# Kernel tuning notes

Measured on AMD Instinct MI355X. Metric: run time of the kernel, lower is better.

The kernel has to match this reference:

```python
import jax, jax.numpy as jnp
import numpy as np

N = 50000      # nodes
E = 800000     # edges (before self loops)
IN_DIM = 128
HID = 16
HEADS = 8
OUT_DIM = 40
NEG_SLOPE = 0.2


def setup_inputs() -> dict:
    key = jax.random.key(0)
    ks = jax.random.split(key, 10)
    x = jax.random.normal(ks[0], (N, IN_DIM), jnp.float32)
    edge_index = jax.random.randint(ks[1], (2, E), 0, N, dtype=jnp.int32)
    # layer 1: GATConv(IN_DIM, HID, heads=HEADS, concat=True)
    W1 = jax.random.normal(ks[2], (IN_DIM, HEADS * HID), jnp.float32) / np.sqrt(IN_DIM).astype(np.float32)
    att_src1 = jax.random.normal(ks[3], (HEADS, HID), jnp.float32) * 0.1
    att_dst1 = jax.random.normal(ks[4], (HEADS, HID), jnp.float32) * 0.1
    bias1 = jnp.zeros((HEADS * HID,), jnp.float32)
    # layer 2: GATConv(HEADS*HID, OUT_DIM, heads=1, concat=False)
    W2 = jax.random.normal(ks[5], (HEADS * HID, OUT_DIM), jnp.float32) / np.sqrt(HEADS * HID).astype(np.float32)
    att_src2 = jax.random.normal(ks[6], (1, OUT_DIM), jnp.float32) * 0.1
    att_dst2 = jax.random.normal(ks[7], (1, OUT_DIM), jnp.float32) * 0.1
    bias2 = jnp.zeros((OUT_DIM,), jnp.float32)
    return {"x": x, "W1": W1, "att_src1": att_src1, "att_dst1": att_dst1, "bias1": bias1,
            "W2": W2, "att_src2": att_src2, "att_dst2": att_dst2, "bias2": bias2,
            "edge_index": edge_index}


def gat_conv(x, src, dst, W, att_src, att_dst, bias, heads, dim, concat, num_nodes):
    # h: [N, H, D]
    h = (x @ W).reshape(num_nodes, heads, dim)
    a_src = jnp.sum(h * att_src, axis=-1)  # [N, H]
    a_dst = jnp.sum(h * att_dst, axis=-1)  # [N, H]
    e = a_src[src] + a_dst[dst]            # [E', H]
    e = jnp.where(e > 0, e, NEG_SLOPE * e)  # leaky_relu
    # segment softmax over edges sharing the same target node
    m = jax.ops.segment_max(e, dst, num_segments=num_nodes)  # [N, H]
    e = jnp.exp(e - m[dst])
    s = jax.ops.segment_sum(e, dst, num_segments=num_nodes)  # [N, H]
    alpha = e / (s[dst] + 1e-16)            # [E', H]
    msg = h[src] * alpha[:, :, None]        # [E', H, D]
    out = jax.ops.segment_sum(msg, dst, num_segments=num_nodes)  # [N, H, D]
    if concat:
        out = out.reshape(num_nodes, heads * dim)
    else:
        out = out.mean(axis=1)
    return out + bias


def reference(x, W1, att_src1, att_dst1, bias1, W2, att_src2, att_dst2, bias2, edge_index):
    # add self loops (PyG GATConv default)
    loop = jnp.arange(N, dtype=edge_index.dtype)
    src = jnp.concatenate([edge_index[0], loop])
    dst = jnp.concatenate([edge_index[1], loop])
    # eval mode: dropout (p=0.6) is identity
    h = gat_conv(x, src, dst, W1, att_src1, att_dst1, bias1, HEADS, HID, True, N)
    h = jax.nn.elu(h)
    out = gat_conv(h, src, dst, W2, att_src2, att_dst2, bias2, 1, OUT_DIM, False, N)
    return jax.nn.log_softmax(out, axis=1)
```

## Files before the change

kernel.cpp:

```cpp
#include <hip/hip_runtime.h>
#include <math.h>

#define IN_DIM 128
#define HEADS 8
#define HID 16
#define OUT_DIM 40
#define NEG 0.2f
#define NSLICE 8

typedef short bf16x8 __attribute__((ext_vector_type(8)));
typedef float f32x4 __attribute__((ext_vector_type(4)));

__device__ __forceinline__ unsigned short f32_to_bf16_rne(float v) {
  unsigned u = __float_as_uint(v);
  return (unsigned short)((u + 0x7FFFu + ((u >> 16) & 1u)) >> 16);
}


__global__ __launch_bounds__(1024) void scanA_k(const int* __restrict__ deg, int* __restrict__ rp,
                                                int* __restrict__ bsum, int n) {
  __shared__ int wsum[16];
  int tid = threadIdx.x;
  int i = blockIdx.x * 1024 + tid;
  int lane = tid & 63, w = tid >> 6;
  int v = (i < n) ? deg[i] : 0;
  int x = v;
  #pragma unroll
  for (int off = 1; off < 64; off <<= 1) {
    int y = __shfl_up(x, off);
    if (lane >= off) x += y;
  }
  if (lane == 63) wsum[w] = x;
  __syncthreads();
  if (tid < 16) {
    int s = wsum[tid];
    #pragma unroll
    for (int off = 1; off < 16; off <<= 1) {
      int y = __shfl_up(s, off);
      if (tid >= off) s += y;
    }
    wsum[tid] = s;
  }
  __syncthreads();
  int woff = (w == 0) ? 0 : wsum[w - 1];
  if (i < n) rp[i] = woff + x - v;
  if (tid == 0) bsum[blockIdx.x] = wsum[15];
}

__global__ __launch_bounds__(1024) void scanB_k(int* __restrict__ bsum, int nb,
                                                int* __restrict__ rp, int n) {
  __shared__ int wsum[16];
  int tid = threadIdx.x;
  int lane = tid & 63, w = tid >> 6;
  int v = (tid < nb) ? bsum[tid] : 0;
  int x = v;
  #pragma unroll
  for (int off = 1; off < 64; off <<= 1) {
    int y = __shfl_up(x, off);
    if (lane >= off) x += y;
  }
  if (lane == 63) wsum[w] = x;
  __syncthreads();
  if (tid < 16) {
    int s = wsum[tid];
    #pragma unroll
    for (int off = 1; off < 16; off <<= 1) {
      int y = __shfl_up(s, off);
      if (tid >= off) s += y;
    }
    wsum[tid] = s;
  }
  __syncthreads();
  int woff = (w == 0) ? 0 : wsum[w - 1];
  if (tid < nb) bsum[tid] = woff + x - v;
  if (tid == 0) rp[n] = wsum[15];
}

__global__ __launch_bounds__(1024) void scanC_k(int* __restrict__ rp, const int* __restrict__ bsum,
                                                int* __restrict__ cnt, int n) {
  int i = blockIdx.x * 1024 + threadIdx.x;
  if (i < n) {
    int v = rp[i] + bsum[blockIdx.x];
    rp[i] = v;
    cnt[i] = v;
  }
}

__global__ void scatter_k(const int* __restrict__ ei, int E0, int N, int snode,
                          int* __restrict__ cnt, int* __restrict__ csr_src) {
  int b = blockIdx.x;
  int slice = b & (NSLICE - 1);
  int e = (b >> 3) * 256 + threadIdx.x;
  int EP = E0 + N;
  if (e >= EP) return;
  int d = (e < E0) ? ei[E0 + e] : (e - E0);
  if (d / snode != slice) return;
  int s = (e < E0) ? ei[e] : d;
  int pos = atomicAdd(&cnt[d], 1);
  csr_src[pos] = s;
}

__global__ void prep_k(const float* __restrict__ W1, const float* __restrict__ as1,
                       const float* __restrict__ ad1, const float* __restrict__ W2,
                       const float* __restrict__ as2, const float* __restrict__ ad2,
                       unsigned short* __restrict__ whi, unsigned short* __restrict__ wlo,
                       unsigned short* __restrict__ w2p, int* __restrict__ deg, int N) {
  int t = blockIdx.x * 256 + threadIdx.x;
  if (t < N) deg[t] = 0;
  if (t < 18432) {
    int j = t & 7, lane = (t >> 3) & 63, kc = (t >> 9) & 3, ct = t >> 11;
    int k = kc * 32 + (lane >> 4) * 8 + j;
    int col = lane & 15;
    float v;
    if (ct < 8) {
      v = W1[k * 128 + ct * 16 + col];
    } else {
      int h = col & 7;
      const float* att = (col < 8) ? as1 : ad1;
      float s = 0.f;
      #pragma unroll
      for (int d = 0; d < 16; ++d) s += W1[k * 128 + h * 16 + d] * att[h * 16 + d];
      v = s;
    }
    unsigned u = __float_as_uint(v);
    unsigned hi = (u + 0x7FFFu + ((u >> 16) & 1u)) >> 16;
    float rem = v - __uint_as_float(hi << 16);
    unsigned ur = __float_as_uint(rem);
    unsigned lo = (ur + 0x7FFFu + ((ur >> 16) & 1u)) >> 16;
    whi[t] = (unsigned short)hi;
    wlo[t] = (unsigned short)lo;
  } else if (t < 18432 + 6144) {
    int u2 = t - 18432;
    int j = u2 & 7, lane = (u2 >> 3) & 63, kc = (u2 >> 9) & 3, ct = u2 >> 11;
    int k = kc * 32 + (lane >> 4) * 8 + j;
    int col = ct * 16 + (lane & 15);
    float v;
    if (col < OUT_DIM) {
      v = W2[k * OUT_DIM + col];
    } else if (col < 42) {
      const float* att = (col == OUT_DIM) ? as2 : ad2;
      float s = 0.f;
      #pragma unroll 8
      for (int d = 0; d < OUT_DIM; ++d) s += W2[k * OUT_DIM + d] * att[d];
      v = s;
    } else {
      v = 0.f;
    }
    w2p[u2] = f32_to_bf16_rne(v);
  }
}

__global__ __launch_bounds__(256) void gemm1_hist_k(
    const float* __restrict__ x, const unsigned short* __restrict__ whi,
    const unsigned short* __restrict__ wlo,
    unsigned short* __restrict__ h1, float* __restrict__ a1s, float* __restrict__ a1d,
    int N, int G1,
    const int* __restrict__ ei, int E0, int snode, int* __restrict__ deg) {
  if ((int)blockIdx.x >= G1) {
    int b = blockIdx.x - G1;
    int slice = b & (NSLICE - 1);
    int e = (b >> 3) * 256 + threadIdx.x;
    int EP = E0 + N;
    if (e >= EP) return;
    int d = (e < E0) ? ei[E0 + e] : (e - E0);
    if (d / snode == slice) atomicAdd(&deg[d], 1);
    return;
  }
  int w = threadIdx.x >> 6, lane = threadIdx.x & 63;
  int quad = lane >> 4, l15 = lane & 15;
  int row = blockIdx.x * 64 + w * 16 + l15;
  int rowc = (row < N) ? row : (N - 1);

  f32x4 acc[9];
  #pragma unroll
  for (int t = 0; t < 9; ++t) acc[t] = (f32x4){0.f, 0.f, 0.f, 0.f};

  const float* xr = x + (size_t)rowc * 128 + quad * 8;
  #pragma unroll
  for (int kc = 0; kc < 4; ++kc) {
    f32x4 a0 = *reinterpret_cast<const f32x4*>(xr + kc * 32);
    f32x4 a1 = *reinterpret_cast<const f32x4*>(xr + kc * 32 + 4);
    float av[8] = {a0.x, a0.y, a0.z, a0.w, a1.x, a1.y, a1.z, a1.w};
    bf16x8 ahi, alo;
    #pragma unroll
    for (int j = 0; j < 8; ++j) {
      unsigned u = __float_as_uint(av[j]);
      unsigned hi = (u + 0x7FFFu + ((u >> 16) & 1u)) >> 16;
      float rem = av[j] - __uint_as_float(hi << 16);
      unsigned ur = __float_as_uint(rem);
      unsigned lo = (ur + 0x7FFFu + ((ur >> 16) & 1u)) >> 16;
      ahi[j] = (short)hi;
      alo[j] = (short)lo;
    }
    #pragma unroll
    for (int ct = 0; ct < 9; ++ct) {
      bf16x8 bh = *reinterpret_cast<const bf16x8*>(whi + ((size_t)(ct * 4 + kc) * 64 + lane) * 8);
      bf16x8 bl = *reinterpret_cast<const bf16x8*>(wlo + ((size_t)(ct * 4 + kc) * 64 + lane) * 8);
      acc[ct] = __builtin_amdgcn_mfma_f32_16x16x32_bf16(ahi, bh, acc[ct], 0, 0, 0);
      acc[ct] = __builtin_amdgcn_mfma_f32_16x16x32_bf16(ahi, bl, acc[ct], 0, 0, 0);
      acc[ct] = __builtin_amdgcn_mfma_f32_16x16x32_bf16(alo, bh, acc[ct], 0, 0, 0);
    }
  }
  int rbase = blockIdx.x * 64 + w * 16 + quad * 4;
  #pragma unroll
  for (int reg = 0; reg < 4; ++reg) {
    int r = rbase + reg;
    if (r < N) {
      #pragma unroll
      for (int ct = 0; ct < 8; ++ct)
        h1[(size_t)r * 128 + ct * 16 + l15] = f32_to_bf16_rne(acc[ct][reg]);
      float v = acc[8][reg];
      if (l15 < 8) a1s[r * 8 + l15] = v;
      else         a1d[r * 8 + (l15 - 8)] = v;
    }
  }
}

__global__ __launch_bounds__(256) void agg1_k(
    const int* __restrict__ row_ptr, const int* __restrict__ csr_src,
    const float* __restrict__ a1s, const float* __restrict__ a1d,
    const unsigned* __restrict__ h1u, const float* __restrict__ bias1,
    unsigned* __restrict__ vrowp, int N) {
  int wid = threadIdx.x >> 6;
  int lane = threadIdx.x & 63;
  int n = blockIdx.x * 4 + wid;

  __shared__ __align__(16) float wls_s[4][8 * 132];
  __shared__ __align__(16) int   srcs_s[4][128];

  if (n >= N) return;
  float* wls  = wls_s[wid];
  int*   srcs = srcs_s[wid];

  int rs = row_ptr[n], re = row_ptr[n + 1];
  int deg = re - rs;
  int h = lane >> 3;

  float accx = 0.f, accy = 0.f, inv;

  if (deg <= 128) {
    for (int i0 = lane; i0 < deg; i0 += 64) srcs[i0] = csr_src[rs + i0];
    int slot = lane >> 3, hw = lane & 7;
    float adn = a1d[n * 8 + hw];
    float sw = 0.f;
    for (int i0 = 0; i0 < deg; i0 += 16) {
      int ia = i0 + slot, ib = i0 + 8 + slot;
      bool va = ia < deg, vb = ib < deg;
      int sa = srcs[va ? ia : 0];
      int sb = srcs[vb ? ib : 0];
      float ea = a1s[sa * 8 + hw] + adn;
      float eb = a1s[sb * 8 + hw] + adn;
      ea = fmaxf(ea, NEG * ea);
      eb = fmaxf(eb, NEG * eb);
      float wa = va ? __expf(ea) : 0.f;
      float wb = vb ? __expf(eb) : 0.f;
      sw += wa + wb;
      if (va) wls[hw * 132 + ia] = wa;
      if (vb) wls[hw * 132 + ib] = wb;
    }
    sw += __shfl_xor(sw, 8);
    sw += __shfl_xor(sw, 16);
    sw += __shfl_xor(sw, 32);
    inv = __shfl(1.f / (sw + 1e-16f), h);

    const float* wh = wls + h * 132;
    int i = 0;
    for (; i + 16 <= deg; i += 16) {
      int4 sa = *reinterpret_cast<const int4*>(srcs + i);
      int4 sb = *reinterpret_cast<const int4*>(srcs + i + 4);
      int4 sc = *reinterpret_cast<const int4*>(srcs + i + 8);
      int4 sd = *reinterpret_cast<const int4*>(srcs + i + 12);
      float4 wa = *reinterpret_cast<const float4*>(wh + i);
      float4 wb = *reinterpret_cast<const float4*>(wh + i + 4);
      float4 wc = *reinterpret_cast<const float4*>(wh + i + 8);
      float4 wd = *reinterpret_cast<const float4*>(wh + i + 12);
      unsigned u0 = h1u[(size_t)sa.x * 64 + lane];
      unsigned u1 = h1u[(size_t)sa.y * 64 + lane];
      unsigned u2 = h1u[(size_t)sa.z * 64 + lane];
      unsigned u3 = h1u[(size_t)sa.w * 64 + lane];
      unsigned u4 = h1u[(size_t)sb.x * 64 + lane];
      unsigned u5 = h1u[(size_t)sb.y * 64 + lane];
      unsigned u6 = h1u[(size_t)sb.z * 64 + lane];
      unsigned u7 = h1u[(size_t)sb.w * 64 + lane];
      unsigned u8 = h1u[(size_t)sc.x * 64 + lane];
      unsigned u9 = h1u[(size_t)sc.y * 64 + lane];
      unsigned uA = h1u[(size_t)sc.z * 64 + lane];
      unsigned uB = h1u[(size_t)sc.w * 64 + lane];
      unsigned uC = h1u[(size_t)sd.x * 64 + lane];
      unsigned uD = h1u[(size_t)sd.y * 64 + lane];
      unsigned uE = h1u[(size_t)sd.z * 64 + lane];
      unsigned uF = h1u[(size_t)sd.w * 64 + lane];
      accx += wa.x * __uint_as_float(u0 << 16) + wa.y * __uint_as_float(u1 << 16)
            + wa.z * __uint_as_float(u2 << 16) + wa.w * __uint_as_float(u3 << 16)
            + wb.x * __uint_as_float(u4 << 16) + wb.y * __uint_as_float(u5 << 16)
            + wb.z * __uint_as_float(u6 << 16) + wb.w * __uint_as_float(u7 << 16)
            + wc.x * __uint_as_float(u8 << 16) + wc.y * __uint_as_float(u9 << 16)
            + wc.z * __uint_as_float(uA << 16) + wc.w * __uint_as_float(uB << 16)
            + wd.x * __uint_as_float(uC << 16) + wd.y * __uint_as_float(uD << 16)
            + wd.z * __uint_as_float(uE << 16) + wd.w * __uint_as_float(uF << 16);
      accy += wa.x * __uint_as_float(u0 & 0xFFFF0000u) + wa.y * __uint_as_float(u1 & 0xFFFF0000u)
            + wa.z * __uint_as_float(u2 & 0xFFFF0000u) + wa.w * __uint_as_float(u3 & 0xFFFF0000u)
            + wb.x * __uint_as_float(u4 & 0xFFFF0000u) + wb.y * __uint_as_float(u5 & 0xFFFF0000u)
            + wb.z * __uint_as_float(u6 & 0xFFFF0000u) + wb.w * __uint_as_float(u7 & 0xFFFF0000u)
            + wc.x * __uint_as_float(u8 & 0xFFFF0000u) + wc.y * __uint_as_float(u9 & 0xFFFF0000u)
            + wc.z * __uint_as_float(uA & 0xFFFF0000u) + wc.w * __uint_as_float(uB & 0xFFFF0000u)
            + wd.x * __uint_as_float(uC & 0xFFFF0000u) + wd.y * __uint_as_float(uD & 0xFFFF0000u)
            + wd.z * __uint_as_float(uE & 0xFFFF0000u) + wd.w * __uint_as_float(uF & 0xFFFF0000u);
    }
    for (; i + 4 <= deg; i += 4) {
      int4 sa = *reinterpret_cast<const int4*>(srcs + i);
      float4 wa = *reinterpret_cast<const float4*>(wh + i);
      unsigned u0 = h1u[(size_t)sa.x * 64 + lane];
      unsigned u1 = h1u[(size_t)sa.y * 64 + lane];
      unsigned u2 = h1u[(size_t)sa.z * 64 + lane];
      unsigned u3 = h1u[(size_t)sa.w * 64 + lane];
      accx += wa.x * __uint_as_float(u0 << 16) + wa.y * __uint_as_float(u1 << 16)
            + wa.z * __uint_as_float(u2 << 16) + wa.w * __uint_as_float(u3 << 16);
      accy += wa.x * __uint_as_float(u0 & 0xFFFF0000u) + wa.y * __uint_as_float(u1 & 0xFFFF0000u)
            + wa.z * __uint_as_float(u2 & 0xFFFF0000u) + wa.w * __uint_as_float(u3 & 0xFFFF0000u);
    }
    for (; i < deg; ++i) {
      int s = srcs[i];
      float w = wh[i];
      unsigned u = h1u[(size_t)s * 64 + lane];
      accx += w * __uint_as_float(u << 16);
      accy += w * __uint_as_float(u & 0xFFFF0000u);
    }
  } else {
    float adn = a1d[n * 8 + h];
    float sw = 0.f;
    for (int i = rs; i < re; ++i) {
      int s = csr_src[i];
      float e = a1s[s * 8 + h] + adn;
      e = fmaxf(e, NEG * e);
      float w = __expf(e);
      unsigned u = h1u[(size_t)s * 64 + lane];
      sw += w;
      accx += w * __uint_as_float(u << 16);
      accy += w * __uint_as_float(u & 0xFFFF0000u);
    }
    inv = 1.f / (sw + 1e-16f);
  }

  float2 b = *reinterpret_cast<const float2*>(bias1 + 2 * lane);
  float vx = accx * inv + b.x;
  float vy = accy * inv + b.y;
  vx = (vx > 0.f) ? vx : (__expf(vx) - 1.f);
  vy = (vy > 0.f) ? vy : (__expf(vy) - 1.f);
  unsigned packed = (unsigned)f32_to_bf16_rne(vx) | ((unsigned)f32_to_bf16_rne(vy) << 16);
  vrowp[(size_t)n * 64 + lane] = packed;
}

__global__ __launch_bounds__(256) void gemm2_mfma_k(
    const unsigned short* __restrict__ vrow, const unsigned short* __restrict__ w2p,
    unsigned short* __restrict__ h2, float* __restrict__ a2s, float* __restrict__ a2d, int N) {
  int w = threadIdx.x >> 6, lane = threadIdx.x & 63;
  int quad = lane >> 4, l15 = lane & 15;
  int row = blockIdx.x * 64 + w * 16 + l15;
  int rowc = (row < N) ? row : (N - 1);

  f32x4 acc[3];
  #pragma unroll
  for (int t = 0; t < 3; ++t) acc[t] = (f32x4){0.f, 0.f, 0.f, 0.f};

  const unsigned short* vr = vrow + (size_t)rowc * 128 + quad * 8;
  #pragma unroll
  for (int kc = 0; kc < 4; ++kc) {
    bf16x8 a = *reinterpret_cast<const bf16x8*>(vr + kc * 32);
    #pragma unroll
    for (int ct = 0; ct < 3; ++ct) {
      bf16x8 bfrag = *reinterpret_cast<const bf16x8*>(w2p + ((size_t)(ct * 4 + kc) * 64 + lane) * 8);
      acc[ct] = __builtin_amdgcn_mfma_f32_16x16x32_bf16(a, bfrag, acc[ct], 0, 0, 0);
    }
  }
  int rbase = blockIdx.x * 64 + w * 16 + quad * 4;
  #pragma unroll
  for (int reg = 0; reg < 4; ++reg) {
    int r = rbase + reg;
    if (r < N) {
      #pragma unroll
      for (int ct = 0; ct < 3; ++ct) {
        int col = ct * 16 + l15;
        float v = acc[ct][reg];
        if (col < OUT_DIM)       h2[(size_t)r * 64 + col] = f32_to_bf16_rne(v);
        else if (col == OUT_DIM) a2s[r] = v;
        else if (col == 41)      a2d[r] = v;
      }
    }
  }
}

__global__ __launch_bounds__(256) void agg2_k(
    const int* __restrict__ row_ptr, const int* __restrict__ csr_src,
    const float* __restrict__ a2s, const float* __restrict__ a2d,
    const unsigned short* __restrict__ h2, const float* __restrict__ bias2,
    float* __restrict__ out, int N) {
  int wid = threadIdx.x >> 6;
  int lane = threadIdx.x & 63;
  int n = blockIdx.x * 4 + wid;

  __shared__ __align__(16) float wls_s[4][128];
  __shared__ __align__(16) int   srcs_s[4][128];

  if (n >= N) return;
  float* wls  = wls_s[wid];
  int*   srcs = srcs_s[wid];

  int rs = row_ptr[n], re = row_ptr[n + 1];
  int deg = re - rs;
  float adn = a2d[n];
  bool act = lane < OUT_DIM;
  float acc = 0.f, inv;

  if (deg <= 128) {
    for (int i0 = lane; i0 < deg; i0 += 64) srcs[i0] = csr_src[rs + i0];
    int ia = lane, ib = lane + 64;
    bool va = ia < deg, vb = ib < deg;
    int sa = srcs[va ? ia : 0];
    int sb = srcs[vb ? ib : 0];
    float ea = a2s[sa] + adn;
    float eb = a2s[sb] + adn;
    ea = fmaxf(ea, NEG * ea);
    eb = fmaxf(eb, NEG * eb);
    float wa = va ? __expf(ea) : 0.f;
    float wb = vb ? __expf(eb) : 0.f;
    float sw = wa + wb;
    if (va) wls[ia] = wa;
    if (vb) wls[ib] = wb;
    #pragma unroll
    for (int off = 32; off > 0; off >>= 1) sw += __shfl_xor(sw, off);
    inv = 1.f / (sw + 1e-16f);

    int i = 0;
    for (; i + 16 <= deg; i += 16) {
      int4 s0 = *reinterpret_cast<const int4*>(srcs + i);
      int4 s1 = *reinterpret_cast<const int4*>(srcs + i + 4);
      int4 s2 = *reinterpret_cast<const int4*>(srcs + i + 8);
      int4 s3 = *reinterpret_cast<const int4*>(srcs + i + 12);
      float4 w0 = *reinterpret_cast<const float4*>(wls + i);
      float4 w1 = *reinterpret_cast<const float4*>(wls + i + 4);
      float4 w2 = *reinterpret_cast<const float4*>(wls + i + 8);
      float4 w3 = *reinterpret_cast<const float4*>(wls + i + 12);
      unsigned g0 = h2[(size_t)s0.x * 64 + lane];
      unsigned g1 = h2[(size_t)s0.y * 64 + lane];
      unsigned g2 = h2[(size_t)s0.z * 64 + lane];
      unsigned g3 = h2[(size_t)s0.w * 64 + lane];
      unsigned g4 = h2[(size_t)s1.x * 64 + lane];
      unsigned g5 = h2[(size_t)s1.y * 64 + lane];
      unsigned g6 = h2[(size_t)s1.z * 64 + lane];
      unsigned g7 = h2[(size_t)s1.w * 64 + lane];
      unsigned g8 = h2[(size_t)s2.x * 64 + lane];
      unsigned g9 = h2[(size_t)s2.y * 64 + lane];
      unsigned gA = h2[(size_t)s2.z * 64 + lane];
      unsigned gB = h2[(size_t)s2.w * 64 + lane];
      unsigned gC = h2[(size_t)s3.x * 64 + lane];
      unsigned gD = h2[(size_t)s3.y * 64 + lane];
      unsigned gE = h2[(size_t)s3.z * 64 + lane];
      unsigned gF = h2[(size_t)s3.w * 64 + lane];
      acc += w0.x * __uint_as_float(g0 << 16) + w0.y * __uint_as_float(g1 << 16)
           + w0.z * __uint_as_float(g2 << 16) + w0.w * __uint_as_float(g3 << 16)
           + w1.x * __uint_as_float(g4 << 16) + w1.y * __uint_as_float(g5 << 16)
           + w1.z * __uint_as_float(g6 << 16) + w1.w * __uint_as_float(g7 << 16)
           + w2.x * __uint_as_float(g8 << 16) + w2.y * __uint_as_float(g9 << 16)
           + w2.z * __uint_as_float(gA << 16) + w2.w * __uint_as_float(gB << 16)
           + w3.x * __uint_as_float(gC << 16) + w3.y * __uint_as_float(gD << 16)
           + w3.z * __uint_as_float(gE << 16) + w3.w * __uint_as_float(gF << 16);
    }
    for (; i + 4 <= deg; i += 4) {
      int4 s0 = *reinterpret_cast<const int4*>(srcs + i);
      float4 w0 = *reinterpret_cast<const float4*>(wls + i);
      unsigned g0 = h2[(size_t)s0.x * 64 + lane];
      unsigned g1 = h2[(size_t)s0.y * 64 + lane];
      unsigned g2 = h2[(size_t)s0.z * 64 + lane];
      unsigned g3 = h2[(size_t)s0.w * 64 + lane];
      acc += w0.x * __uint_as_float(g0 << 16) + w0.y * __uint_as_float(g1 << 16)
           + w0.z * __uint_as_float(g2 << 16) + w0.w * __uint_as_float(g3 << 16);
    }
    for (; i < deg; ++i) {
      int s = srcs[i];
      float w = wls[i];
      unsigned g = h2[(size_t)s * 64 + lane];
      acc += w * __uint_as_float(g << 16);
    }
  } else {
    float sw = 0.f;
    for (int i = rs; i < re; ++i) {
      int s = csr_src[i];
      float e = a2s[s] + adn;
      e = fmaxf(e, NEG * e);
      float w = __expf(e);
      sw += w;
      unsigned g = h2[(size_t)s * 64 + lane];
      acc += w * __uint_as_float(g << 16);
    }
    inv = 1.f / (sw + 1e-16f);
  }

  float v = act ? (acc * inv + bias2[lane]) : -1e30f;
  float vm = v;
  #pragma unroll
  for (int off = 32; off > 0; off >>= 1) vm = fmaxf(vm, __shfl_xor(vm, off));
  float ex = act ? __expf(v - vm) : 0.f;
  float es = ex;
  #pragma unroll
  for (int off = 32; off > 0; off >>= 1) es += __shfl_xor(es, off);
  if (act) out[(size_t)n * OUT_DIM + lane] = v - vm - __logf(es);
}


extern "C" void kernel_launch(void* const* d_in, const int* in_sizes, int n_in,
                              void* d_out, int out_size, void* d_ws, size_t ws_size,
                              hipStream_t stream) {
  const float* x   = (const float*)d_in[0];
  const float* W1  = (const float*)d_in[1];
  const float* as1 = (const float*)d_in[2];
  const float* ad1 = (const float*)d_in[3];
  const float* b1  = (const float*)d_in[4];
  const float* W2  = (const float*)d_in[5];
  const float* as2 = (const float*)d_in[6];
  const float* ad2 = (const float*)d_in[7];
  const float* b2  = (const float*)d_in[8];
  const int*   ei  = (const int*)d_in[9];
  int N  = in_sizes[0] / IN_DIM;
  int E0 = in_sizes[9] / 2;
  int EP = E0 + N;
  int snode = (N + NSLICE - 1) / NSLICE;
  float* out = (float*)d_out;

  char* ws = (char*)d_ws;
  size_t off = 0;
  auto alloc = [&](size_t bytes) {
    char* p = ws + off;
    off += (bytes + 255) & ~size_t(255);
    return p;
  };
  unsigned short* h1   = (unsigned short*)alloc((size_t)N * 128 * 2);
  float* a1s  = (float*)alloc((size_t)N * 8 * 4);
  float* a1d  = (float*)alloc((size_t)N * 8 * 4);
  unsigned*       vrow = (unsigned*)alloc((size_t)N * 64 * 4);
  unsigned short* h2   = (unsigned short*)alloc((size_t)N * 64 * 2);
  float* a2s  = (float*)alloc((size_t)N * 4);
  float* a2d  = (float*)alloc((size_t)N * 4);
  int*   deg  = (int*)alloc((size_t)N * 4);
  int*   cnt  = (int*)alloc((size_t)N * 4);
  int*   rp   = (int*)alloc((size_t)(N + 4) * 4);
  int*   bsum = (int*)alloc((size_t)1024 * 4);
  int*   csr  = (int*)alloc((size_t)EP * 4);
  unsigned short* whi = (unsigned short*)alloc((size_t)18432 * 2);
  unsigned short* wlo = (unsigned short*)alloc((size_t)18432 * 2);
  unsigned short* w2p = (unsigned short*)alloc((size_t)6144 * 2);

  int nb = (N + 1023) / 1024;
  int nchunk = (EP + 255) / 256;
  int G1 = (N + 63) / 64;
  prep_k<<<(N + 255) / 256, 256, 0, stream>>>(W1, as1, ad1, W2, as2, ad2, whi, wlo, w2p, deg, N);
  gemm1_hist_k<<<G1 + nchunk * NSLICE, 256, 0, stream>>>(x, whi, wlo, h1, a1s, a1d, N, G1,
                                                         ei, E0, snode, deg);
  scanA_k<<<nb, 1024, 0, stream>>>(deg, rp, bsum, N);
  scanB_k<<<1, 1024, 0, stream>>>(bsum, nb, rp, N);
  scanC_k<<<nb, 1024, 0, stream>>>(rp, bsum, cnt, N);
  scatter_k<<<nchunk * NSLICE, 256, 0, stream>>>(ei, E0, N, snode, cnt, csr);
  agg1_k<<<(N + 3) / 4, 256, 0, stream>>>(rp, csr, a1s, a1d, (const unsigned*)h1, b1, vrow, N);
  gemm2_mfma_k<<<(N + 63) / 64, 256, 0, stream>>>((const unsigned short*)vrow, w2p, h2, a2s, a2d, N);
  agg2_k<<<(N + 3) / 4, 256, 0, stream>>>(rp, csr, a2s, a2d, h2, b2, out, N);
}
```

Measured before the change: 258.0 us.

## Reschedule CSR build: histogram in prep, fuse scans, scatter alongside gemm1, pair-gather agg2

```diff
diff --git a/kernel.cpp b/kernel.cpp
--- a/kernel.cpp
+++ b/kernel.cpp
@@ -7,6 +7,7 @@
 #define OUT_DIM 40
 #define NEG 0.2f
 #define NSLICE 8
+#define PREP_BLOCKS 96
 
 typedef short bf16x8 __attribute__((ext_vector_type(8)));
 typedef float f32x4 __attribute__((ext_vector_type(4)));
@@ -16,97 +17,24 @@
   return (unsigned short)((u + 0x7FFFu + ((u >> 16) & 1u)) >> 16);
 }
 
-
-__global__ __launch_bounds__(1024) void scanA_k(const int* __restrict__ deg, int* __restrict__ rp,
-                                                int* __restrict__ bsum, int n) {
-  __shared__ int wsum[16];
-  int tid = threadIdx.x;
-  int i = blockIdx.x * 1024 + tid;
-  int lane = tid & 63, w = tid >> 6;
-  int v = (i < n) ? deg[i] : 0;
-  int x = v;
-  #pragma unroll
-  for (int off = 1; off < 64; off <<= 1) {
-    int y = __shfl_up(x, off);
-    if (lane >= off) x += y;
-  }
-  if (lane == 63) wsum[w] = x;
-  __syncthreads();
-  if (tid < 16) {
-    int s = wsum[tid];
-    #pragma unroll
-    for (int off = 1; off < 16; off <<= 1) {
-      int y = __shfl_up(s, off);
-      if (tid >= off) s += y;
-    }
-    wsum[tid] = s;
-  }
-  __syncthreads();
-  int woff = (w == 0) ? 0 : wsum[w - 1];
-  if (i < n) rp[i] = woff + x - v;
-  if (tid == 0) bsum[blockIdx.x] = wsum[15];
-}
-
-__global__ __launch_bounds__(1024) void scanB_k(int* __restrict__ bsum, int nb,
-                                                int* __restrict__ rp, int n) {
-  __shared__ int wsum[16];
-  int tid = threadIdx.x;
-  int lane = tid & 63, w = tid >> 6;
-  int v = (tid < nb) ? bsum[tid] : 0;
-  int x = v;
-  #pragma unroll
-  for (int off = 1; off < 64; off <<= 1) {
-    int y = __shfl_up(x, off);
-    if (lane >= off) x += y;
-  }
-  if (lane == 63) wsum[w] = x;
-  __syncthreads();
-  if (tid < 16) {
-    int s = wsum[tid];
-    #pragma unroll
-    for (int off = 1; off < 16; off <<= 1) {
-      int y = __shfl_up(s, off);
-      if (tid >= off) s += y;
-    }
-    wsum[tid] = s;
-  }
-  __syncthreads();
-  int woff = (w == 0) ? 0 : wsum[w - 1];
-  if (tid < nb) bsum[tid] = woff + x - v;
-  if (tid == 0) rp[n] = wsum[15];
-}
-
-__global__ __launch_bounds__(1024) void scanC_k(int* __restrict__ rp, const int* __restrict__ bsum,
-                                                int* __restrict__ cnt, int n) {
-  int i = blockIdx.x * 1024 + threadIdx.x;
-  if (i < n) {
-    int v = rp[i] + bsum[blockIdx.x];
-    rp[i] = v;
-    cnt[i] = v;
-  }
-}
-
-__global__ void scatter_k(const int* __restrict__ ei, int E0, int N, int snode,
-                          int* __restrict__ cnt, int* __restrict__ csr_src) {
-  int b = blockIdx.x;
-  int slice = b & (NSLICE - 1);
-  int e = (b >> 3) * 256 + threadIdx.x;
-  int EP = E0 + N;
-  if (e >= EP) return;
-  int d = (e < E0) ? ei[E0 + e] : (e - E0);
-  if (d / snode != slice) return;
-  int s = (e < E0) ? ei[e] : d;
-  int pos = atomicAdd(&cnt[d], 1);
-  csr_src[pos] = s;
-}
-
-__global__ void prep_k(const float* __restrict__ W1, const float* __restrict__ as1,
-                       const float* __restrict__ ad1, const float* __restrict__ W2,
-                       const float* __restrict__ as2, const float* __restrict__ ad2,
-                       unsigned short* __restrict__ whi, unsigned short* __restrict__ wlo,
-                       unsigned short* __restrict__ w2p, int* __restrict__ deg, int N) {
+__global__ void prep_hist_k(const float* __restrict__ W1, const float* __restrict__ as1,
+                            const float* __restrict__ ad1, const float* __restrict__ W2,
+                            const float* __restrict__ as2, const float* __restrict__ ad2,
+                            unsigned short* __restrict__ whi, unsigned short* __restrict__ wlo,
+                            unsigned short* __restrict__ w2p,
+                            const int* __restrict__ ei, int E0, int N, int snode,
+                            int* __restrict__ deg) {
+  if ((int)blockIdx.x >= PREP_BLOCKS) {
+    int b = blockIdx.x - PREP_BLOCKS;
+    int slice = b & (NSLICE - 1);
+    int e = (b >> 3) * 256 + threadIdx.x;
+    int EP = E0 + N;
+    if (e >= EP) return;
+    int d = (e < E0) ? ei[E0 + e] : (e - E0);
+    if (d / snode == slice) atomicAdd(&deg[d], 1);
+    return;
+  }
   int t = blockIdx.x * 256 + threadIdx.x;
-  if (t < N) deg[t] = 0;
   if (t < 18432) {
     int j = t & 7, lane = (t >> 3) & 63, kc = (t >> 9) & 3, ct = t >> 11;
     int k = kc * 32 + (lane >> 4) * 8 + j;
@@ -150,12 +78,82 @@
   }
 }
 
-__global__ __launch_bounds__(256) void gemm1_hist_k(
+__global__ __launch_bounds__(1024) void scanA_k(const int* __restrict__ deg, int* __restrict__ rp,
+                                                int* __restrict__ bsum, int n) {
+  __shared__ int wsum[16];
+  int tid = threadIdx.x;
+  int i = blockIdx.x * 1024 + tid;
+  int lane = tid & 63, w = tid >> 6;
+  int v = (i < n) ? deg[i] : 0;
+  int x = v;
+  #pragma unroll
+  for (int off = 1; off < 64; off <<= 1) {
+    int y = __shfl_up(x, off);
+    if (lane >= off) x += y;
+  }
+  if (lane == 63) wsum[w] = x;
+  __syncthreads();
+  if (tid < 16) {
+    int s = wsum[tid];
+    #pragma unroll
+    for (int off = 1; off < 16; off <<= 1) {
+      int y = __shfl_up(s, off);
+      if (tid >= off) s += y;
+    }
+    wsum[tid] = s;
+  }
+  __syncthreads();
+  int woff = (w == 0) ? 0 : wsum[w - 1];
+  if (i < n) rp[i] = woff + x - v;
+  if (tid == 0) bsum[blockIdx.x] = wsum[15];
+}
+
+__global__ __launch_bounds__(1024) void scanBC_k(const int* __restrict__ bsum, int nb,
+                                                 int* __restrict__ rp, int* __restrict__ cnt, int n) {
+  __shared__ int wsum[16];
+  __shared__ int offs[1025];
+  int tid = threadIdx.x;
+  int lane = tid & 63, w = tid >> 6;
+  int v = (tid < nb) ? bsum[tid] : 0;
+  int x = v;
+  #pragma unroll
+  for (int off = 1; off < 64; off <<= 1) {
+    int y = __shfl_up(x, off);
+    if (lane >= off) x += y;
+  }
+  if (lane == 63) wsum[w] = x;
+  __syncthreads();
+  if (tid < 16) {
+    int s = wsum[tid];
+    #pragma unroll
+    for (int off = 1; off < 16; off <<= 1) {
+      int y = __shfl_up(s, off);
+      if (tid >= off) s += y;
+    }
+    wsum[tid] = s;
+  }
+  __syncthreads();
+  int woff = (w == 0) ? 0 : wsum[w - 1];
+  if (tid < nb) offs[tid + 1] = woff + x;
+  if (tid == 0) offs[0] = 0;
+  __syncthreads();
+  int add = offs[blockIdx.x];
+  int i = blockIdx.x * 1024 + tid;
+  if (i < n) {
+    int val = rp[i] + add;
+    rp[i] = val;
+    cnt[i] = val;
+  }
+  if (blockIdx.x == 0 && tid == 0) rp[n] = offs[nb];
+}
+
+__global__ __launch_bounds__(256) void gemm1_scatter_k(
     const float* __restrict__ x, const unsigned short* __restrict__ whi,
     const unsigned short* __restrict__ wlo,
     unsigned short* __restrict__ h1, float* __restrict__ a1s, float* __restrict__ a1d,
     int N, int G1,
-    const int* __restrict__ ei, int E0, int snode, int* __restrict__ deg) {
+    const int* __restrict__ ei, int E0, int snode,
+    int* __restrict__ cnt, int* __restrict__ csr_src) {
   if ((int)blockIdx.x >= G1) {
     int b = blockIdx.x - G1;
     int slice = b & (NSLICE - 1);
@@ -163,7 +161,10 @@
     int EP = E0 + N;
     if (e >= EP) return;
     int d = (e < E0) ? ei[E0 + e] : (e - E0);
-    if (d / snode == slice) atomicAdd(&deg[d], 1);
+    if (d / snode != slice) return;
+    int s = (e < E0) ? ei[e] : d;
+    int pos = atomicAdd(&cnt[d], 1);
+    csr_src[pos] = s;
     return;
   }
   int w = threadIdx.x >> 6, lane = threadIdx.x & 63;
@@ -393,7 +394,7 @@
 __global__ __launch_bounds__(256) void agg2_k(
     const int* __restrict__ row_ptr, const int* __restrict__ csr_src,
     const float* __restrict__ a2s, const float* __restrict__ a2d,
-    const unsigned short* __restrict__ h2, const float* __restrict__ bias2,
+    const unsigned* __restrict__ h2u, const float* __restrict__ bias2,
     float* __restrict__ out, int N) {
   int wid = threadIdx.x >> 6;
   int lane = threadIdx.x & 63;
@@ -409,8 +410,9 @@
   int rs = row_ptr[n], re = row_ptr[n + 1];
   int deg = re - rs;
   float adn = a2d[n];
-  bool act = lane < OUT_DIM;
-  float acc = 0.f, inv;
+  int pair = lane >> 5;
+  int c32  = lane & 31;
+  float accx = 0.f, accy = 0.f, inv;
 
   if (deg <= 128) {
     for (int i0 = lane; i0 < deg; i0 += 64) srcs[i0] = csr_src[rs + i0];
@@ -433,78 +435,62 @@
 
     int i = 0;
     for (; i + 16 <= deg; i += 16) {
-      int4 s0 = *reinterpret_cast<const int4*>(srcs + i);
-      int4 s1 = *reinterpret_cast<const int4*>(srcs + i + 4);
-      int4 s2 = *reinterpret_cast<const int4*>(srcs + i + 8);
-      int4 s3 = *reinterpret_cast<const int4*>(srcs + i + 12);
-      float4 w0 = *reinterpret_cast<const float4*>(wls + i);
-      float4 w1 = *reinterpret_cast<const float4*>(wls + i + 4);
-      float4 w2 = *reinterpret_cast<const float4*>(wls + i + 8);
-      float4 w3 = *reinterpret_cast<const float4*>(wls + i + 12);
-      unsigned g0 = h2[(size_t)s0.x * 64 + lane];
-      unsigned g1 = h2[(size_t)s0.y * 64 + lane];
-      unsigned g2 = h2[(size_t)s0.z * 64 + lane];
-      unsigned g3 = h2[(size_t)s0.w * 64 + lane];
-      unsigned g4 = h2[(size_t)s1.x * 64 + lane];
-      unsigned g5 = h2[(size_t)s1.y * 64 + lane];
-      unsigned g6 = h2[(size_t)s1.z * 64 + lane];
-      unsigned g7 = h2[(size_t)s1.w * 64 + lane];
-      unsigned g8 = h2[(size_t)s2.x * 64 + lane];
-      unsigned g9 = h2[(size_t)s2.y * 64 + lane];
-      unsigned gA = h2[(size_t)s2.z * 64 + lane];
-      unsigned gB = h2[(size_t)s2.w * 64 + lane];
-      unsigned gC = h2[(size_t)s3.x * 64 + lane];
-      unsigned gD = h2[(size_t)s3.y * 64 + lane];
-      unsigned gE = h2[(size_t)s3.z * 64 + lane];
-      unsigned gF = h2[(size_t)s3.w * 64 + lane];
-      acc += w0.x * __uint_as_float(g0 << 16) + w0.y * __uint_as_float(g1 << 16)
-           + w0.z * __uint_as_float(g2 << 16) + w0.w * __uint_as_float(g3 << 16)
-           + w1.x * __uint_as_float(g4 << 16) + w1.y * __uint_as_float(g5 << 16)
-           + w1.z * __uint_as_float(g6 << 16) + w1.w * __uint_as_float(g7 << 16)
-           + w2.x * __uint_as_float(g8 << 16) + w2.y * __uint_as_float(g9 << 16)
-           + w2.z * __uint_as_float(gA << 16) + w2.w * __uint_as_float(gB << 16)
-           + w3.x * __uint_as_float(gC << 16) + w3.y * __uint_as_float(gD << 16)
-           + w3.z * __uint_as_float(gE << 16) + w3.w * __uint_as_float(gF << 16);
-    }
-    for (; i + 4 <= deg; i += 4) {
-      int4 s0 = *reinterpret_cast<const int4*>(srcs + i);
-      float4 w0 = *reinterpret_cast<const float4*>(wls + i);
-      unsigned g0 = h2[(size_t)s0.x * 64 + lane];
-      unsigned g1 = h2[(size_t)s0.y * 64 + lane];
-      unsigned g2 = h2[(size_t)s0.z * 64 + lane];
-      unsigned g3 = h2[(size_t)s0.w * 64 + lane];
-      acc += w0.x * __uint_as_float(g0 << 16) + w0.y * __uint_as_float(g1 << 16)
-           + w0.z * __uint_as_float(g2 << 16) + w0.w * __uint_as_float(g3 << 16);
-    }
-    for (; i < deg; ++i) {
-      int s = srcs[i];
-      float w = wls[i];
-      unsigned g = h2[(size_t)s * 64 + lane];
-      acc += w * __uint_as_float(g << 16);
+      #pragma unroll
+      for (int j = 0; j < 8; ++j) {
+        int idx = i + 2 * j + pair;
+        int s = srcs[idx];
+        float w = wls[idx];
+        unsigned g = h2u[(size_t)s * 32 + c32];
+        accx += w * __uint_as_float(g << 16);
+        accy += w * __uint_as_float(g & 0xFFFF0000u);
+      }
+    }
+    for (; i < deg; i += 2) {
+      int idx = i + pair;
+      bool val = idx < deg;
+      int s = srcs[val ? idx : 0];
+      float w = val ? wls[idx] : 0.f;
+      unsigned g = h2u[(size_t)s * 32 + c32];
+      accx += w * __uint_as_float(g << 16);
+      accy += w * __uint_as_float(g & 0xFFFF0000u);
     }
   } else {
     float sw = 0.f;
-    for (int i = rs; i < re; ++i) {
-      int s = csr_src[i];
+    for (int i = rs; i < re; i += 2) {
+      int idx = i + pair;
+      bool val = idx < re;
+      int s = csr_src[val ? idx : rs];
       float e = a2s[s] + adn;
       e = fmaxf(e, NEG * e);
-      float w = __expf(e);
+      float w = val ? __expf(e) : 0.f;
       sw += w;
-      unsigned g = h2[(size_t)s * 64 + lane];
-      acc += w * __uint_as_float(g << 16);
-    }
-    inv = 1.f / (sw + 1e-16f);
-  }
-
-  float v = act ? (acc * inv + bias2[lane]) : -1e30f;
-  float vm = v;
+      unsigned g = h2u[(size_t)s * 32 + c32];
+      accx += w * __uint_as_float(g << 16);
+      accy += w * __uint_as_float(g & 0xFFFF0000u);
+    }
+    #pragma unroll
+    for (int off = 32; off > 0; off >>= 1) sw += __shfl_xor(sw, off);
+    inv = 32.f / (sw + 1e-16f);
+  }
+
+  accx += __shfl_xor(accx, 32);
+  accy += __shfl_xor(accy, 32);
+  int c0 = 2 * c32, c1 = 2 * c32 + 1;
+  bool a0 = (lane < 32) && (c0 < OUT_DIM);
+  bool a1 = (lane < 32) && (c1 < OUT_DIM);
+  float v0 = a0 ? (accx * inv + bias2[c0]) : -1e30f;
+  float v1 = a1 ? (accy * inv + bias2[c1]) : -1e30f;
+  float vm = fmaxf(v0, v1);
   #pragma unroll
   for (int off = 32; off > 0; off >>= 1) vm = fmaxf(vm, __shfl_xor(vm, off));
-  float ex = act ? __expf(v - vm) : 0.f;
-  float es = ex;
-  #pragma unroll
-  for (int off = 32; off > 0; off >>= 1) es += __shfl_xor(es, off);
-  if (act) out[(size_t)n * OUT_DIM + lane] = v - vm - __logf(es);
+  float ex = (a0 ? __expf(v0 - vm) : 0.f) + (a1 ? __expf(v1 - vm) : 0.f);
+  #pragma unroll
+  for (int off = 32; off > 0; off >>= 1) ex += __shfl_xor(ex, off);
+  if (lane < OUT_DIM / 2) {
+    float le = __logf(ex);
+    float2 o = make_float2(v0 - vm - le, v1 - vm - le);
+    *reinterpret_cast<float2*>(out + (size_t)n * OUT_DIM + c0) = o;
+  }
 }
 
 
@@ -553,14 +539,15 @@
   int nb = (N + 1023) / 1024;
   int nchunk = (EP + 255) / 256;
   int G1 = (N + 63) / 64;
-  prep_k<<<(N + 255) / 256, 256, 0, stream>>>(W1, as1, ad1, W2, as2, ad2, whi, wlo, w2p, deg, N);
-  gemm1_hist_k<<<G1 + nchunk * NSLICE, 256, 0, stream>>>(x, whi, wlo, h1, a1s, a1d, N, G1,
-                                                         ei, E0, snode, deg);
+
+  hipMemsetAsync(deg, 0, (size_t)N * 4, stream);
+  prep_hist_k<<<PREP_BLOCKS + nchunk * NSLICE, 256, 0, stream>>>(
+      W1, as1, ad1, W2, as2, ad2, whi, wlo, w2p, ei, E0, N, snode, deg);
   scanA_k<<<nb, 1024, 0, stream>>>(deg, rp, bsum, N);
-  scanB_k<<<1, 1024, 0, stream>>>(bsum, nb, rp, N);
-  scanC_k<<<nb, 1024, 0, stream>>>(rp, bsum, cnt, N);
-  scatter_k<<<nchunk * NSLICE, 256, 0, stream>>>(ei, E0, N, snode, cnt, csr);
+  scanBC_k<<<nb, 1024, 0, stream>>>(bsum, nb, rp, cnt, N);
+  gemm1_scatter_k<<<G1 + nchunk * NSLICE, 256, 0, stream>>>(
+      x, whi, wlo, h1, a1s, a1d, N, G1, ei, E0, snode, cnt, csr);
   agg1_k<<<(N + 3) / 4, 256, 0, stream>>>(rp, csr, a1s, a1d, (const unsigned*)h1, b1, vrow, N);
-  gemm2_mfma_k<<<(N + 63) / 64, 256, 0, stream>>>((const unsigned short*)vrow, w2p, h2, a2s, a2d, N);
-  agg2_k<<<(N + 3) / 4, 256, 0, stream>>>(rp, csr, a2s, a2d, h2, b2, out, N);
-}
+  gemm2_mfma_k<<<G1, 256, 0, stream>>>((const unsigned short*)vrow, w2p, h2, a2s, a2d, N);
+  agg2_k<<<(N + 3) / 4, 256, 0, stream>>>(rp, csr, a2s, a2d, (const unsigned*)h2, b2, out, N);
+}
```

After: 263.8 us. +2.3%, slower.
